# Kernel tuning notes

Measured on AMD Instinct MI355X. Metric: run time of the kernel, lower is better.

The kernel has to match this reference:

```python
import jax, jax.numpy as jnp
import numpy as np

H = 8
NUM_GRAPHS = 128
EDGE_DIM = 147

def _glorot(k, shape, fan_in):
    return jax.random.normal(k, shape, jnp.float32) * (1.0 / np.sqrt(fan_in))

def setup_inputs():
    ks = jax.random.split(jax.random.key(0), 28)
    N, E = 50000, 200000
    inp = {}
    inp['x'] = jax.random.normal(ks[0], (N, 64), jnp.float32)
    inp['edge_attr'] = jax.random.uniform(ks[1], (E, EDGE_DIM), dtype=jnp.float32)
    dims = [(64, 64), (512, 64), (512, 32)]  # (in_channels, per-head out) per GATConv layer
    ki = 2
    for i in range(3):
        cin, c = dims[i]
        hc = H * c
        inp['W%d' % i] = _glorot(ks[ki], (hc, cin), cin); ki += 1
        inp['We%d' % i] = _glorot(ks[ki], (hc, EDGE_DIM), EDGE_DIM); ki += 1
        inp['as%d' % i] = _glorot(ks[ki], (1, H, c), c); ki += 1
        inp['ad%d' % i] = _glorot(ks[ki], (1, H, c), c); ki += 1
        inp['ae%d' % i] = _glorot(ks[ki], (1, H, c), c); ki += 1
        inp['b%d' % i] = jnp.zeros((hc,), jnp.float32); ki += 1
    inp['Wc'] = _glorot(ks[ki], (32, 256), 256)
    inp['bc'] = jnp.zeros((32,), jnp.float32)
    inp['edge_index'] = jax.random.randint(ks[ki + 1], (2, E), 0, N)
    inp['batch'] = jnp.sort(jax.random.randint(ks[ki + 2], (N,), 0, NUM_GRAPHS))
    return inp

def _gat_layer(x, src, dst, ea, W, We, a_s, a_d, a_e, b):
    # PyG GATConv (concat=True, eval mode): project, per-edge attention logits,
    # softmax over incoming edges of each destination node, weighted scatter-sum, bias.
    N = x.shape[0]
    HC = W.shape[0]
    C = HC // H
    xp = (x @ W.T).reshape(N, H, C)              # [N,H,C]
    ep = (ea @ We.T).reshape(-1, H, C)           # [E,H,C]
    logits = (xp * a_s).sum(-1)[src] + (xp * a_d).sum(-1)[dst] + (ep * a_e).sum(-1)
    logits = jax.nn.leaky_relu(logits, 0.2)      # [E,H]
    mx = jax.ops.segment_max(logits, dst, num_segments=N)
    mx = jnp.where(jnp.isfinite(mx), mx, 0.0)
    ex = jnp.exp(logits - mx[dst])
    denom = jax.ops.segment_sum(ex, dst, num_segments=N)
    attn = ex / (denom[dst] + 1e-16)             # [E,H]
    out = jax.ops.segment_sum(xp[src] * attn[:, :, None], dst, num_segments=N)
    return out.reshape(N, HC) + b

def _forward(x, edge_attr, params, Wc, bc, edge_index, batch):
    N = x.shape[0]
    src, dst = edge_index[0], edge_index[1]
    # GATConv add_self_loops=True, fill_value='mean': self-loop edge attr is
    # the per-node mean of incoming edge attrs (0 for isolated nodes).
    ones_e = jnp.ones((src.shape[0],), x.dtype)
    deg = jax.ops.segment_sum(ones_e, dst, num_segments=N)
    loop_attr = jax.ops.segment_sum(edge_attr, dst, num_segments=N) / jnp.clip(deg, 1.0)[:, None]
    ar = jnp.arange(N)
    src_f = jnp.concatenate([src, ar])
    dst_f = jnp.concatenate([dst, ar])
    ea_f = jnp.concatenate([edge_attr, loop_attr], axis=0)
    h = x
    for i, p in enumerate(params):
        h = _gat_layer(h, src_f, dst_f, ea_f, *p)
        if i < len(params) - 1:
            h = jax.nn.elu(h)  # dropout is identity in eval
    # batch indices are sorted and contiguous, so the unique->contiguous remap
    # in the original forward is the identity; global mean pool:
    cnt = jax.ops.segment_sum(jnp.ones((N,), h.dtype), batch, num_segments=NUM_GRAPHS)
    pooled = jax.ops.segment_sum(h, batch, num_segments=NUM_GRAPHS) / jnp.clip(cnt, 1.0)[:, None]
    return pooled @ Wc.T + bc

def reference(x, edge_attr, W0, We0, as0, ad0, ae0, b0, W1, We1, as1, ad1, ae1, b1, W2, We2, as2, ad2, ae2, b2, Wc, bc, edge_index, batch):
    params = [(W0, We0, as0, ad0, ae0, b0), (W1, We1, as1, ad1, ae1, b1), (W2, We2, as2, ad2, ae2, b2)]
    return _forward(x, edge_attr, params, Wc, bc, edge_index, batch)
```

## Files before the change

### kernel.cpp

```cpp
#include <hip/hip_runtime.h>
#include <hip/hip_bf16.h>
#include <math.h>

typedef __attribute__((ext_vector_type(8))) _Float16 f16x8;
typedef __attribute__((ext_vector_type(4))) _Float16 f16x4;
typedef __attribute__((ext_vector_type(4))) float f32x4;

#define AS1(p) ((const __attribute__((address_space(1))) void*)(p))
#define AS3(p) ((__attribute__((address_space(3))) void*)(p))

__device__ __forceinline__ float leaky02(float x){ return x > 0.f ? x : 0.2f*x; }
__device__ __forceinline__ ushort f2h(float f){ _Float16 h = (_Float16)f; return *(ushort*)&h; }
__device__ __forceinline__ float h2f(ushort u){ _Float16 h = *(_Float16*)&u; return (float)h; }

__global__ void count_kernel(const int* __restrict__ dst, int* __restrict__ cnt, int E){
  int e = blockIdx.x*blockDim.x + threadIdx.x;
  if (e < E) atomicAdd(&cnt[dst[e]], 1);
}

__global__ void scanA_kernel(const int* __restrict__ cnt, int* __restrict__ bsum, int N){
  __shared__ int sd[256];
  int i = blockIdx.x*256 + threadIdx.x;
  sd[threadIdx.x] = (i<N) ? cnt[i] : 0;
  __syncthreads();
  for (int off=128; off>0; off>>=1){
    if (threadIdx.x < off) sd[threadIdx.x] += sd[threadIdx.x+off];
    __syncthreads();
  }
  if (threadIdx.x==0) bsum[blockIdx.x] = sd[0];
}
__global__ void scanB_kernel(int* __restrict__ bsum, int B){
  __shared__ int sd[256];
  int t = threadIdx.x;
  int v = (t<B) ? bsum[t] : 0;
  sd[t] = v;
  __syncthreads();
  for (int off=1; off<256; off<<=1){
    int u = (t>=off) ? sd[t-off] : 0;
    __syncthreads();
    sd[t] += u;
    __syncthreads();
  }
  if (t<B) bsum[t] = sd[t] - v;
}
__global__ void scanC_kernel(const int* __restrict__ cnt, const int* __restrict__ bsum,
                             int* __restrict__ row_ptr, int N){
  __shared__ int sd[256];
  int i = blockIdx.x*256 + threadIdx.x;
  int v = (i<N) ? cnt[i] : 0;
  sd[threadIdx.x] = v;
  __syncthreads();
  for (int off=1; off<256; off<<=1){
    int u = (threadIdx.x>=off) ? sd[threadIdx.x-off] : 0;
    __syncthreads();
    sd[threadIdx.x] += u;
    __syncthreads();
  }
  if (i < N) row_ptr[i+1] = sd[threadIdx.x] + bsum[blockIdx.x];
  if (i == 0) row_ptr[0] = 0;
}

__global__ void scatter_kernel(const int* __restrict__ dst, const int* __restrict__ row_ptr,
                               int* __restrict__ cursor, int* __restrict__ csr, int E){
  int e = blockIdx.x*blockDim.x + threadIdx.x;
  if (e < E){
    int d = dst[e];
    int pos = row_ptr[d] + atomicAdd(&cursor[d], 1);
    csr[pos] = e;
  }
}

__global__ void conv4_kernel(const float* __restrict__ p0, const float* __restrict__ p1,
                             const float* __restrict__ p2, const float* __restrict__ p3,
                             ushort* __restrict__ q0, ushort* __restrict__ q1,
                             ushort* __restrict__ q2, ushort* __restrict__ q3,
                             int n0, int n1, int n2, int n3){
  int i = blockIdx.x*256 + threadIdx.x;
  const float* src; ushort* dst; int loc;
  if (i < n0){ src=p0; dst=q0; loc=i; }
  else if (i < n0+n1){ src=p1; dst=q1; loc=i-n0; }
  else if (i < n0+n1+n2){ src=p2; dst=q2; loc=i-n0-n1; }
  else if (i < n0+n1+n2+n3){ src=p3; dst=q3; loc=i-n0-n1-n2; }
  else return;
  float4 v = reinterpret_cast<const float4*>(src)[loc];
  ushort4 o; o.x=f2h(v.x); o.y=f2h(v.y); o.z=f2h(v.z); o.w=f2h(v.w);
  reinterpret_cast<ushort4*>(dst)[loc] = o;
}

__global__ void wfold_direct_kernel(const float* __restrict__ We0, const float* __restrict__ ae0,
                                    const float* __restrict__ We1, const float* __restrict__ ae1,
                                    const float* __restrict__ We2, const float* __restrict__ ae2,
                                    ushort* __restrict__ Bh){
  int t = blockIdx.x*256 + threadIdx.x;
  if (t >= 32*160) return;
  int j = t/160, d = t%160;
  float s = 0.f;
  if (j < 24 && d < 147){
    int l = j >> 3, h = j & 7;
    const float* We = (l==0) ? We0 : (l==1) ? We1 : We2;
    const float* ae = (l==0) ? ae0 : (l==1) ? ae1 : ae2;
    int C = (l==2) ? 32 : 64;
    for (int c=0;c<C;c++) s = fmaf(We[(size_t)(h*C+c)*147 + d], ae[h*C+c], s);
  }
  Bh[t] = f2h(s);
}

__global__ __launch_bounds__(256) void edge_alpha_mfma_kernel(const float* __restrict__ ea, const ushort* __restrict__ Bh,
                                                              float* __restrict__ alphaE, int E){
  int wave = threadIdx.x>>6, lane = threadIdx.x&63;
  int fr = lane&15, fq = lane>>4;
  int m0 = blockIdx.x*64 + wave*16;
  f32x4 acc0 = {0.f,0.f,0.f,0.f}, acc1 = {0.f,0.f,0.f,0.f};
  int row = m0 + fr; if (row > E-1) row = E-1;
  const float*  ar = ea + (size_t)row*147;
  const ushort* b0 = Bh + (size_t)fr*160      + fq*8;
  const ushort* b1 = Bh + (size_t)(16+fr)*160 + fq*8;
  #pragma unroll
  for (int k=0;k<160;k+=32){
    int c0 = k + fq*8;
    f16x8 a;
    #pragma unroll
    for (int u=0;u<8;u++){
      float v = (c0+u < 147) ? ar[c0+u] : 0.f;
      a[u] = (_Float16)v;
    }
    f16x8 p = *(const f16x8*)(b0 + k);
    f16x8 q = *(const f16x8*)(b1 + k);
    acc0 = __builtin_amdgcn_mfma_f32_16x16x32_f16(a, p, acc0, 0, 0, 0);
    acc1 = __builtin_amdgcn_mfma_f32_16x16x32_f16(a, q, acc1, 0, 0, 0);
  }
  #pragma unroll
  for (int j=0;j<4;j++){
    int r = m0 + fq*4 + j;
    if (r < E){
      alphaE[(size_t)r*24 + fr] = acc0[j];
      if (fr < 8) alphaE[(size_t)r*24 + 16 + fr] = acc1[j];
    }
  }
}

__global__ __launch_bounds__(192) void loop_alpha_all_kernel(const float* __restrict__ alphaE, const int* __restrict__ row_ptr,
                                                             const int* __restrict__ csr, float* __restrict__ loopAE, int N){
  int n = blockIdx.x*8 + threadIdx.x/24;
  int j = threadIdx.x%24;
  if (n >= N) return;
  int row = row_ptr[n], end = row_ptr[n+1];
  float s = 0.f;
  for (int i=row;i<end;i++) s += alphaE[(size_t)csr[i]*24 + j];
  loopAE[(size_t)n*24 + j] = s / fmaxf((float)(end-row), 1.0f);
}

template<int CPH>
__global__ __launch_bounds__(256) void gemm_mfma_kernel(const ushort* __restrict__ A, const ushort* __restrict__ B,
                                                        ushort* __restrict__ C,
                                                        const float* __restrict__ a_s, const float* __restrict__ a_d,
                                                        float* __restrict__ alphaS, float* __restrict__ alphaD,
                                                        int M, int Nn, int K, int NY){
  __shared__ ushort lds[128*64*4];
  int nwg = gridDim.x;
  int bid = blockIdx.x;
  int q8 = nwg >> 3, r8 = nwg & 7;
  int xcd = bid & 7, loc = bid >> 3;
  int swz = (xcd < r8 ? xcd*(q8+1) : r8*(q8+1) + (xcd-r8)*q8) + loc;
  int m0 = (swz / NY) * 128, n0 = (swz % NY) * 128;

  int wave = threadIdx.x >> 6, lane = threadIdx.x & 63;
  int wr = wave >> 1, wc = wave & 1;
  f32x4 acc[4][4];
  #pragma unroll
  for (int m=0;m<4;m++)
    #pragma unroll
    for (int n=0;n<4;n++) acc[m][n] = (f32x4){0.f,0.f,0.f,0.f};

  int lrow = lane >> 3;
  int lcol = lane & 7;
  int srcChunk = lcol ^ lrow;
  int fr = lane & 15;
  int fq = lane >> 4;

  auto stage = [&](int buf, int k0){
    ushort* As = lds + buf*(128*64*2);
    ushort* Bs = As + 128*64;
    #pragma unroll
    for (int qq=0;qq<4;qq++){
      int r = qq*32 + wave*8 + lrow;
      int gr = m0 + r; if (gr > M-1) gr = M-1;
      __builtin_amdgcn_global_load_lds(AS1(A + (size_t)gr*K + k0 + srcChunk*8), AS3(&As[(qq*32 + wave*8)*64]), 16, 0, 0);
      __builtin_amdgcn_global_load_lds(AS1(B + (size_t)(n0 + r)*K + k0 + srcChunk*8), AS3(&Bs[(qq*32 + wave*8)*64]), 16, 0, 0);
    }
  };

  int nt = K >> 6;
  stage(0, 0);
  int buf = 0;
  for (int t=0; t<nt; ++t){
    if (t+1 < nt){
      stage(buf^1, (t+1)<<6);
      asm volatile("s_waitcnt vmcnt(8)" ::: "memory");
    } else {
      asm volatile("s_waitcnt vmcnt(0)" ::: "memory");
    }
    __builtin_amdgcn_s_barrier();
    __builtin_amdgcn_sched_barrier(0);
    const ushort* As = lds + buf*(128*64*2);
    const ushort* Bs = As + 128*64;
    #pragma unroll
    for (int kk=0; kk<64; kk+=32){
      f16x8 a[4], b[4];
      #pragma unroll
      for (int m=0;m<4;m++){
        int Ra = wr*64 + m*16 + fr;
        int ch = ((kk>>3) + fq) ^ (Ra & 7);
        a[m] = *(const f16x8*)&As[Ra*64 + ch*8];
      }
      #pragma unroll
      for (int n=0;n<4;n++){
        int Rb = wc*64 + n*16 + fr;
        int ch = ((kk>>3) + fq) ^ (Rb & 7);
        b[n] = *(const f16x8*)&Bs[Rb*64 + ch*8];
      }
      #pragma unroll
      for (int m=0;m<4;m++)
        #pragma unroll
        for (int n=0;n<4;n++)
          acc[m][n] = __builtin_amdgcn_mfma_f32_16x16x32_f16(a[m], b[n], acc[m][n], 0, 0, 0);
    }
    __builtin_amdgcn_s_barrier();
    buf ^= 1;
  }

  {
    ushort* Cs = lds;
    #pragma unroll
    for (int m=0;m<4;m++)
      #pragma unroll
      for (int j=0;j<4;j++){
        int rr = wr*64 + m*16 + fq*4 + j;
        #pragma unroll
        for (int n=0;n<4;n++)
          Cs[rr*128 + wc*64 + n*16 + fr] = f2h(acc[m][n][j]);
      }
    __builtin_amdgcn_s_barrier();
    int rbase = threadIdx.x >> 4;
    int cc = (threadIdx.x & 15)*8;
    #pragma unroll
    for (int p=0;p<8;p++){
      int rr = p*16 + rbase;
      int grow = m0 + rr;
      if (grow < M)
        *(f16x8*)(C + (size_t)grow*Nn + n0 + cc) = *(const f16x8*)&Cs[rr*128 + cc];
    }
  }

  int colbase = n0 + wc*64;
  if (CPH == 64){
    int head = colbase >> 6;
    float asv[4], adv[4];
    #pragma unroll
    for (int n=0;n<4;n++){ int cih = n*16 + fr; asv[n] = a_s[head*64 + cih]; adv[n] = a_d[head*64 + cih]; }
    #pragma unroll
    for (int m=0;m<4;m++){
      float ps[4] = {0,0,0,0}, pd[4] = {0,0,0,0};
      #pragma unroll
      for (int n=0;n<4;n++)
        #pragma unroll
        for (int j=0;j<4;j++){ ps[j] = fmaf(acc[m][n][j], asv[n], ps[j]); pd[j] = fmaf(acc[m][n][j], adv[n], pd[j]); }
      #pragma unroll
      for (int off=1; off<16; off<<=1)
        #pragma unroll
        for (int j=0;j<4;j++){ ps[j] += __shfl_xor(ps[j], off); pd[j] += __shfl_xor(pd[j], off); }
      if (fr == 0){
        #pragma unroll
        for (int j=0;j<4;j++){
          int row = m0 + wr*64 + m*16 + fq*4 + j;
          if (row < M){ alphaS[(size_t)row*8 + head] = ps[j]; alphaD[(size_t)row*8 + head] = pd[j]; }
        }
      }
    }
  } else {
    int head0 = colbase >> 5;
    float asv[4], adv[4];
    #pragma unroll
    for (int n=0;n<4;n++){
      int h = head0 + (n>>1);
      int cih = (n&1)*16 + fr;
      asv[n] = a_s[h*32 + cih]; adv[n] = a_d[h*32 + cih];
    }
    #pragma unroll
    for (int m=0;m<4;m++){
      float psA[4]={0,0,0,0}, pdA[4]={0,0,0,0}, psB[4]={0,0,0,0}, pdB[4]={0,0,0,0};
      #pragma unroll
      for (int j=0;j<4;j++){
        #pragma unroll
        for (int n=0;n<2;n++){ psA[j] = fmaf(acc[m][n][j], asv[n], psA[j]); pdA[j] = fmaf(acc[m][n][j], adv[n], pdA[j]); }
        #pragma unroll
        for (int n=2;n<4;n++){ psB[j] = fmaf(acc[m][n][j], asv[n], psB[j]); pdB[j] = fmaf(acc[m][n][j], adv[n], pdB[j]); }
      }
      #pragma unroll
      for (int off=1; off<16; off<<=1)
        #pragma unroll
        for (int j=0;j<4;j++){
          psA[j] += __shfl_xor(psA[j], off); pdA[j] += __shfl_xor(pdA[j], off);
          psB[j] += __shfl_xor(psB[j], off); pdB[j] += __shfl_xor(pdB[j], off);
        }
      if (fr == 0){
        #pragma unroll
        for (int j=0;j<4;j++){
          int row = m0 + wr*64 + m*16 + fq*4 + j;
          if (row < M){
            alphaS[(size_t)row*8 + head0]     = psA[j]; alphaD[(size_t)row*8 + head0]     = pdA[j];
            alphaS[(size_t)row*8 + head0 + 1] = psB[j]; alphaD[(size_t)row*8 + head0 + 1] = pdB[j];
          }
        }
      }
    }
  }
}

template<int HC, int ELU>
__global__ __launch_bounds__(256) void aggregate_kernel(
    const ushort* __restrict__ xh, const float* __restrict__ alphaS, const float* __restrict__ alphaD,
    const float* __restrict__ alphaE, const float* __restrict__ loopAE,
    const int* __restrict__ row_ptr, const int* __restrict__ csr, const int* __restrict__ src,
    const float* __restrict__ bias, ushort* __restrict__ out, int N){
  constexpr int V = HC/64;
  int n = blockIdx.x*4 + (threadIdx.x>>6);
  if (n >= N) return;
  int lane = threadIdx.x & 63;
  int h = lane >> 3;
  float adn = alphaD[(size_t)n*8 + h];
  float ls = leaky02(alphaS[(size_t)n*8 + h] + adn + loopAE[(size_t)n*24 + h]);
  float ex = __expf(ls);
  float denom = ex;
  float acc[V];
  {
    const ushort* xr = xh + (size_t)n*HC + V*lane;
    if (V == 8){
      f16x8 v = *(const f16x8*)xr;
      #pragma unroll
      for (int j=0;j<8;j++) acc[j] = ex * (float)v[j];
    } else {
      f16x4 v = *(const f16x4*)xr;
      #pragma unroll
      for (int j=0;j<V;j++) acc[j] = ex * (float)v[j];
    }
  }
  int i = row_ptr[n], i1 = row_ptr[n+1];
  for (; i+1 < i1; i += 2){
    int e0 = csr[i], e1 = csr[i+1];
    int s0 = src[e0], s1 = src[e1];
    float aS0 = alphaS[(size_t)s0*8 + h], aE0 = alphaE[(size_t)e0*24 + h];
    float aS1 = alphaS[(size_t)s1*8 + h], aE1 = alphaE[(size_t)e1*24 + h];
    const ushort* x0 = xh + (size_t)s0*HC + V*lane;
    const ushort* x1 = xh + (size_t)s1*HC + V*lane;
    if (V == 8){
      f16x8 v0 = *(const f16x8*)x0;
      f16x8 v1 = *(const f16x8*)x1;
      float ex0 = __expf(leaky02(aS0 + adn + aE0));
      float ex1 = __expf(leaky02(aS1 + adn + aE1));
      denom += ex0 + ex1;
      #pragma unroll
      for (int j=0;j<8;j++) acc[j] = fmaf(ex1, (float)v1[j], fmaf(ex0, (float)v0[j], acc[j]));
    } else {
      f16x4 v0 = *(const f16x4*)x0;
      f16x4 v1 = *(const f16x4*)x1;
      float ex0 = __expf(leaky02(aS0 + adn + aE0));
      float ex1 = __expf(leaky02(aS1 + adn + aE1));
      denom += ex0 + ex1;
      #pragma unroll
      for (int j=0;j<V;j++) acc[j] = fmaf(ex1, (float)v1[j], fmaf(ex0, (float)v0[j], acc[j]));
    }
  }
  if (i < i1){
    int e = csr[i]; int s = src[e];
    float t = leaky02(alphaS[(size_t)s*8 + h] + adn + alphaE[(size_t)e*24 + h]);
    float exv = __expf(t);
    denom += exv;
    const ushort* xs = xh + (size_t)s*HC + V*lane;
    if (V == 8){
      f16x8 v = *(const f16x8*)xs;
      #pragma unroll
      for (int j=0;j<8;j++) acc[j] = fmaf(exv, (float)v[j], acc[j]);
    } else {
      f16x4 v = *(const f16x4*)xs;
      #pragma unroll
      for (int j=0;j<V;j++) acc[j] = fmaf(exv, (float)v[j], acc[j]);
    }
  }
  float inv = 1.f/(denom + 1e-16f);
  if (V == 8){
    f16x8 ov;
    #pragma unroll
    for (int j=0;j<8;j++){
      float o = acc[j]*inv + bias[V*lane + j];
      if (ELU) o = (o > 0.f) ? o : expm1f(o);
      ov[j] = (_Float16)o;
    }
    *(f16x8*)(out + (size_t)n*HC + V*lane) = ov;
  } else {
    f16x4 ov;
    #pragma unroll
    for (int j=0;j<V;j++){
      float o = acc[j]*inv + bias[V*lane + j];
      if (ELU) o = (o > 0.f) ? o : expm1f(o);
      ov[j] = (_Float16)o;
    }
    *(f16x4*)(out + (size_t)n*HC + V*lane) = ov;
  }
}

__global__ __launch_bounds__(256) void pool_sum_kernel(const ushort* __restrict__ h, const int* __restrict__ batch,
                                                       float* __restrict__ pooled, int N){
  __shared__ int bsh[128];
  int i0 = blockIdx.x*128;
  int i1 = min(i0+128, N);
  if (threadIdx.x < i1-i0) bsh[threadIdx.x] = batch[i0+threadIdx.x];
  __syncthreads();
  int c = threadIdx.x;
  int gprev = bsh[0];
  float s = 0.f;
  for (int i=i0;i<i1;i++){
    int g = bsh[i-i0];
    if (g != gprev){ atomicAdd(&pooled[gprev*256 + c], s); s = 0.f; gprev = g; }
    s += h2f(h[(size_t)i*256 + c]);
  }
  atomicAdd(&pooled[gprev*256 + c], s);
}

__device__ __forceinline__ int lower_bound_i(const int* a, int n, int key){
  int lo=0, hi=n;
  while (lo<hi){ int mid=(lo+hi)>>1; if (a[mid]<key) lo=mid+1; else hi=mid; }
  return lo;
}

__global__ void final_kernel(const float* __restrict__ pooled, const int* __restrict__ batch,
                             const float* __restrict__ Wc, const float* __restrict__ bc,
                             float* __restrict__ out, int N){
  int g = blockIdx.x; int j = threadIdx.x;
  if (j >= 32) return;
  int start = lower_bound_i(batch, N, g);
  int end   = lower_bound_i(batch, N, g+1);
  float invc = 1.f / fmaxf((float)(end-start), 1.f);
  const float* p = pooled + g*256;
  const float* w = Wc + (size_t)j*256;
  float s = 0.f;
  for (int c=0;c<256;c++) s = fmaf(p[c], w[c], s);
  out[g*32 + j] = s*invc + bc[j];
}

extern "C" void kernel_launch(void* const* d_in, const int* in_sizes, int n_in,
                              void* d_out, int out_size, void* d_ws, size_t ws_size,
                              hipStream_t stream){
  (void)n_in; (void)out_size; (void)ws_size;
  const float* x   = (const float*)d_in[0];
  const float* ea  = (const float*)d_in[1];
  const float* Wt[3]  = {(const float*)d_in[2],  (const float*)d_in[8],  (const float*)d_in[14]};
  const float* Wet[3] = {(const float*)d_in[3],  (const float*)d_in[9],  (const float*)d_in[15]};
  const float* ast[3] = {(const float*)d_in[4],  (const float*)d_in[10], (const float*)d_in[16]};
  const float* adt[3] = {(const float*)d_in[5],  (const float*)d_in[11], (const float*)d_in[17]};
  const float* aet[3] = {(const float*)d_in[6],  (const float*)d_in[12], (const float*)d_in[18]};
  const float* bt[3]  = {(const float*)d_in[7],  (const float*)d_in[13], (const float*)d_in[19]};
  const float* Wc  = (const float*)d_in[20];
  const float* bc  = (const float*)d_in[21];
  const int* ei    = (const int*)d_in[22];
  const int* batch = (const int*)d_in[23];
  int N = in_sizes[0] / 64;
  int E = in_sizes[1] / 147;
  const int* srcp = ei;
  const int* dstp = ei + E;

  char* w = (char*)d_ws;
  size_t off = 0;
  auto carve = [&](size_t bytes)->char*{ char* p = w + off; off += (bytes + 255) & ~(size_t)255; return p; };
  ushort* xh     = (ushort*)carve((size_t)N*512*2);
  ushort* hb     = (ushort*)carve((size_t)N*512*2);
  ushort* xb     = (ushort*)carve((size_t)N*64*2);
  ushort* Wb[3];
  Wb[0] = (ushort*)carve((size_t)512*64*2);
  Wb[1] = (ushort*)carve((size_t)512*512*2);
  Wb[2] = (ushort*)carve((size_t)256*512*2);
  ushort* wfBh   = (ushort*)carve((size_t)32*160*2);
  float*  alphaE = (float*) carve((size_t)E*24*4);
  float*  loopAE = (float*) carve((size_t)N*24*4);
  float*  alphaS = (float*) carve((size_t)N*8*4);
  float*  alphaD = (float*) carve((size_t)N*8*4);
  int*    row_ptr= (int*)   carve((size_t)(N+1)*4);
  int*    csr    = (int*)   carve((size_t)E*4);
  int*    bsum   = (int*)   carve((size_t)256*4);
  char*   zbase  = carve(0);
  float*  pooled = (float*) carve((size_t)128*256*4);
  int*    cnt    = (int*)   carve((size_t)N*4);
  int*    cursor = (int*)   carve((size_t)N*4);
  char*   zend   = carve(0);

  hipMemsetAsync(zbase, 0, (size_t)(zend - zbase), stream);

  int nscan = (N+255)/256;
  count_kernel  <<<(E+255)/256, 256, 0, stream>>>(dstp, cnt, E);
  scanA_kernel  <<<nscan, 256, 0, stream>>>(cnt, bsum, N);
  scanB_kernel  <<<1, 256, 0, stream>>>(bsum, nscan);
  scanC_kernel  <<<nscan, 256, 0, stream>>>(cnt, bsum, row_ptr, N);
  scatter_kernel<<<(E+255)/256, 256, 0, stream>>>(dstp, row_ptr, cursor, csr, E);

  wfold_direct_kernel<<<(32*160+255)/256, 256, 0, stream>>>(Wet[0], aet[0], Wet[1], aet[1], Wet[2], aet[2], wfBh);

  conv4_kernel<<<(N*16 + 8192 + 65536 + 32768 + 255)/256, 256, 0, stream>>>(
      x, Wt[0], Wt[1], Wt[2], xb, Wb[0], Wb[1], Wb[2], N*16, 8192, 65536, 32768);

  edge_alpha_mfma_kernel<<<(E+63)/64, 256, 0, stream>>>(ea, wfBh, alphaE, E);
  loop_alpha_all_kernel <<<(N+7)/8, 192, 0, stream>>>(alphaE, row_ptr, csr, loopAE, N);

  const int HCs[3]  = {512, 512, 256};
  const int CINs[3] = {64, 512, 512};
  int nrow = (N+127)/128;
  for (int l=0; l<3; l++){
    int HC = HCs[l], CIN = CINs[l];
    const ushort* Ain = (l==0) ? xb : hb;
    int NY = HC/128;
    int nwg = nrow * NY;
    if (HC==512) gemm_mfma_kernel<64><<<nwg, 256, 0, stream>>>(Ain, Wb[l], xh, ast[l], adt[l], alphaS, alphaD, N, HC, CIN, NY);
    else         gemm_mfma_kernel<32><<<nwg, 256, 0, stream>>>(Ain, Wb[l], xh, ast[l], adt[l], alphaS, alphaD, N, HC, CIN, NY);
    int ablocks = (N + 3) / 4;
    if (l==0)
      aggregate_kernel<512,1><<<ablocks, 256, 0, stream>>>(xh, alphaS, alphaD, alphaE + 0*8, loopAE + 0*8, row_ptr, csr, srcp, bt[l], hb, N);
    else if (l==1)
      aggregate_kernel<512,1><<<ablocks, 256, 0, stream>>>(xh, alphaS, alphaD, alphaE + 1*8, loopAE + 1*8, row_ptr, csr, srcp, bt[l], hb, N);
    else
      aggregate_kernel<256,0><<<ablocks, 256, 0, stream>>>(xh, alphaS, alphaD, alphaE + 2*8, loopAE + 2*8, row_ptr, csr, srcp, bt[l], hb, N);
  }
  pool_sum_kernel<<<(N+127)/128, 256, 0, stream>>>(hb, batch, pooled, N);
  final_kernel<<<128, 64, 0, stream>>>(pooled, batch, Wc, bc, (float*)d_out, N);
}
```

Baseline: 476.7 us.

## Store edge attention in CSR order and precompute per-edge exponentials

The scatter step now records each edge's CSR position and writes the source and destination ids in CSR order. The edge-alpha kernel writes its results straight into CSR order, so the loop-attribute and aggregation kernels read contiguous data instead of following csr→edge indirection. A new per-layer edge_exp kernel computes the leaky-ReLU plus exp for every edge and self loop before aggregation, so the aggregate kernel only loads these values. The cost is an extra kernel launch per layer and an E×8 float buffer written and read each layer, while scattered writes move into the edge-alpha kernel.

New measurement: 487.7 us. 2.3% more time.

```diff
diff --git a/kernel.cpp b/kernel.cpp
--- a/kernel.cpp
+++ b/kernel.cpp
@@ -60,13 +60,17 @@
   if (i == 0) row_ptr[0] = 0;
 }
 
-__global__ void scatter_kernel(const int* __restrict__ dst, const int* __restrict__ row_ptr,
-                               int* __restrict__ cursor, int* __restrict__ csr, int E){
+__global__ void scatter_kernel(const int* __restrict__ src, const int* __restrict__ dst,
+                               const int* __restrict__ row_ptr, int* __restrict__ cursor,
+                               int* __restrict__ epos, int* __restrict__ csr_src,
+                               int* __restrict__ csr_dst, int E){
   int e = blockIdx.x*blockDim.x + threadIdx.x;
   if (e < E){
     int d = dst[e];
     int pos = row_ptr[d] + atomicAdd(&cursor[d], 1);
-    csr[pos] = e;
+    epos[e] = pos;
+    csr_src[pos] = src[e];
+    csr_dst[pos] = d;
   }
 }
 
@@ -106,7 +110,8 @@
 }
 
 __global__ __launch_bounds__(256) void edge_alpha_mfma_kernel(const float* __restrict__ ea, const ushort* __restrict__ Bh,
-                                                              float* __restrict__ alphaE, int E){
+                                                              const int* __restrict__ epos,
+                                                              float* __restrict__ aEc, int E){
   int wave = threadIdx.x>>6, lane = threadIdx.x&63;
   int fr = lane&15, fq = lane>>4;
   int m0 = blockIdx.x*64 + wave*16;
@@ -133,21 +138,42 @@
   for (int j=0;j<4;j++){
     int r = m0 + fq*4 + j;
     if (r < E){
-      alphaE[(size_t)r*24 + fr] = acc0[j];
-      if (fr < 8) alphaE[(size_t)r*24 + 16 + fr] = acc1[j];
-    }
-  }
-}
-
-__global__ __launch_bounds__(192) void loop_alpha_all_kernel(const float* __restrict__ alphaE, const int* __restrict__ row_ptr,
-                                                             const int* __restrict__ csr, float* __restrict__ loopAE, int N){
+      int p = epos[r];
+      aEc[(size_t)p*24 + fr] = acc0[j];
+      if (fr < 8) aEc[(size_t)p*24 + 16 + fr] = acc1[j];
+    }
+  }
+}
+
+__global__ __launch_bounds__(192) void loop_alpha_all_kernel(const float* __restrict__ aEc, const int* __restrict__ row_ptr,
+                                                             float* __restrict__ loopAE, int N){
   int n = blockIdx.x*8 + threadIdx.x/24;
   int j = threadIdx.x%24;
   if (n >= N) return;
   int row = row_ptr[n], end = row_ptr[n+1];
   float s = 0.f;
-  for (int i=row;i<end;i++) s += alphaE[(size_t)csr[i]*24 + j];
+  for (int i=row;i<end;i++) s += aEc[(size_t)i*24 + j];
   loopAE[(size_t)n*24 + j] = s / fmaxf((float)(end-row), 1.0f);
+}
+
+__global__ __launch_bounds__(256) void edge_exp_kernel(
+    const float* __restrict__ alphaS, const float* __restrict__ alphaD,
+    const float* __restrict__ aEc, const float* __restrict__ loopAE,
+    const int* __restrict__ csr_src, const int* __restrict__ csr_dst,
+    float* __restrict__ exv_csr, float* __restrict__ selfEx,
+    int E, int N, int off){
+  int t = blockIdx.x*256 + threadIdx.x;
+  if (t < E*8){
+    int i = t >> 3, h = t & 7;
+    int s = csr_src[i], n = csr_dst[i];
+    float v = leaky02(alphaS[(size_t)s*8+h] + alphaD[(size_t)n*8+h] + aEc[(size_t)i*24 + off + h]);
+    exv_csr[t] = __expf(v);
+  } else if (t < (E+N)*8){
+    int u = t - E*8;
+    int n = u >> 3, h = u & 7;
+    float v = leaky02(alphaS[(size_t)n*8+h] + alphaD[(size_t)n*8+h] + loopAE[(size_t)n*24 + off + h]);
+    selfEx[u] = __expf(v);
+  }
 }
 
 template<int CPH>
@@ -319,18 +345,15 @@
 
 template<int HC, int ELU>
 __global__ __launch_bounds__(256) void aggregate_kernel(
-    const ushort* __restrict__ xh, const float* __restrict__ alphaS, const float* __restrict__ alphaD,
-    const float* __restrict__ alphaE, const float* __restrict__ loopAE,
-    const int* __restrict__ row_ptr, const int* __restrict__ csr, const int* __restrict__ src,
+    const ushort* __restrict__ xh, const float* __restrict__ exv_csr, const float* __restrict__ selfEx,
+    const int* __restrict__ row_ptr, const int* __restrict__ csr_src,
     const float* __restrict__ bias, ushort* __restrict__ out, int N){
   constexpr int V = HC/64;
   int n = blockIdx.x*4 + (threadIdx.x>>6);
   if (n >= N) return;
   int lane = threadIdx.x & 63;
   int h = lane >> 3;
-  float adn = alphaD[(size_t)n*8 + h];
-  float ls = leaky02(alphaS[(size_t)n*8 + h] + adn + loopAE[(size_t)n*24 + h]);
-  float ex = __expf(ls);
+  float ex = selfEx[(size_t)n*8 + h];
   float denom = ex;
   float acc[V];
   {
@@ -347,34 +370,27 @@
   }
   int i = row_ptr[n], i1 = row_ptr[n+1];
   for (; i+1 < i1; i += 2){
-    int e0 = csr[i], e1 = csr[i+1];
-    int s0 = src[e0], s1 = src[e1];
-    float aS0 = alphaS[(size_t)s0*8 + h], aE0 = alphaE[(size_t)e0*24 + h];
-    float aS1 = alphaS[(size_t)s1*8 + h], aE1 = alphaE[(size_t)e1*24 + h];
+    int s0 = csr_src[i], s1 = csr_src[i+1];
+    float ex0 = exv_csr[(size_t)i*8 + h];
+    float ex1 = exv_csr[(size_t)(i+1)*8 + h];
     const ushort* x0 = xh + (size_t)s0*HC + V*lane;
     const ushort* x1 = xh + (size_t)s1*HC + V*lane;
+    denom += ex0 + ex1;
     if (V == 8){
       f16x8 v0 = *(const f16x8*)x0;
       f16x8 v1 = *(const f16x8*)x1;
-      float ex0 = __expf(leaky02(aS0 + adn + aE0));
-      float ex1 = __expf(leaky02(aS1 + adn + aE1));
-      denom += ex0 + ex1;
       #pragma unroll
       for (int j=0;j<8;j++) acc[j] = fmaf(ex1, (float)v1[j], fmaf(ex0, (float)v0[j], acc[j]));
     } else {
       f16x4 v0 = *(const f16x4*)x0;
       f16x4 v1 = *(const f16x4*)x1;
-      float ex0 = __expf(leaky02(aS0 + adn + aE0));
-      float ex1 = __expf(leaky02(aS1 + adn + aE1));
-      denom += ex0 + ex1;
       #pragma unroll
       for (int j=0;j<V;j++) acc[j] = fmaf(ex1, (float)v1[j], fmaf(ex0, (float)v0[j], acc[j]));
     }
   }
   if (i < i1){
-    int e = csr[i]; int s = src[e];
-    float t = leaky02(alphaS[(size_t)s*8 + h] + adn + alphaE[(size_t)e*24 + h]);
-    float exv = __expf(t);
+    int s = csr_src[i];
+    float exv = exv_csr[(size_t)i*8 + h];
     denom += exv;
     const ushort* xs = xh + (size_t)s*HC + V*lane;
     if (V == 8){
@@ -480,12 +496,16 @@
   Wb[1] = (ushort*)carve((size_t)512*512*2);
   Wb[2] = (ushort*)carve((size_t)256*512*2);
   ushort* wfBh   = (ushort*)carve((size_t)32*160*2);
-  float*  alphaE = (float*) carve((size_t)E*24*4);
+  float*  aEc    = (float*) carve((size_t)E*24*4);
   float*  loopAE = (float*) carve((size_t)N*24*4);
   float*  alphaS = (float*) carve((size_t)N*8*4);
   float*  alphaD = (float*) carve((size_t)N*8*4);
+  float*  exv    = (float*) carve((size_t)E*8*4);
+  float*  selfEx = (float*) carve((size_t)N*8*4);
   int*    row_ptr= (int*)   carve((size_t)(N+1)*4);
-  int*    csr    = (int*)   carve((size_t)E*4);
+  int*    epos   = (int*)   carve((size_t)E*4);
+  int*    csr_src= (int*)   carve((size_t)E*4);
+  int*    csr_dst= (int*)   carve((size_t)E*4);
   int*    bsum   = (int*)   carve((size_t)256*4);
   char*   zbase  = carve(0);
   float*  pooled = (float*) carve((size_t)128*256*4);
@@ -500,19 +520,20 @@
   scanA_kernel  <<<nscan, 256, 0, stream>>>(cnt, bsum, N);
   scanB_kernel  <<<1, 256, 0, stream>>>(bsum, nscan);
   scanC_kernel  <<<nscan, 256, 0, stream>>>(cnt, bsum, row_ptr, N);
-  scatter_kernel<<<(E+255)/256, 256, 0, stream>>>(dstp, row_ptr, cursor, csr, E);
+  scatter_kernel<<<(E+255)/256, 256, 0, stream>>>(srcp, dstp, row_ptr, cursor, epos, csr_src, csr_dst, E);
 
   wfold_direct_kernel<<<(32*160+255)/256, 256, 0, stream>>>(Wet[0], aet[0], Wet[1], aet[1], Wet[2], aet[2], wfBh);
 
   conv4_kernel<<<(N*16 + 8192 + 65536 + 32768 + 255)/256, 256, 0, stream>>>(
       x, Wt[0], Wt[1], Wt[2], xb, Wb[0], Wb[1], Wb[2], N*16, 8192, 65536, 32768);
 
-  edge_alpha_mfma_kernel<<<(E+63)/64, 256, 0, stream>>>(ea, wfBh, alphaE, E);
-  loop_alpha_all_kernel <<<(N+7)/8, 192, 0, stream>>>(alphaE, row_ptr, csr, loopAE, N);
+  edge_alpha_mfma_kernel<<<(E+63)/64, 256, 0, stream>>>(ea, wfBh, epos, aEc, E);
+  loop_alpha_all_kernel <<<(N+7)/8, 192, 0, stream>>>(aEc, row_ptr, loopAE, N);
 
   const int HCs[3]  = {512, 512, 256};
   const int CINs[3] = {64, 512, 512};
   int nrow = (N+127)/128;
+  int nexp = ((E+N)*8 + 255)/256;
   for (int l=0; l<3; l++){
     int HC = HCs[l], CIN = CINs[l];
     const ushort* Ain = (l==0) ? xb : hb;
@@ -520,13 +541,14 @@
     int nwg = nrow * NY;
     if (HC==512) gemm_mfma_kernel<64><<<nwg, 256, 0, stream>>>(Ain, Wb[l], xh, ast[l], adt[l], alphaS, alphaD, N, HC, CIN, NY);
     else         gemm_mfma_kernel<32><<<nwg, 256, 0, stream>>>(Ain, Wb[l], xh, ast[l], adt[l], alphaS, alphaD, N, HC, CIN, NY);
+    edge_exp_kernel<<<nexp, 256, 0, stream>>>(alphaS, alphaD, aEc, loopAE, csr_src, csr_dst, exv, selfEx, E, N, l*8);
     int ablocks = (N + 3) / 4;
     if (l==0)
-      aggregate_kernel<512,1><<<ablocks, 256, 0, stream>>>(xh, alphaS, alphaD, alphaE + 0*8, loopAE + 0*8, row_ptr, csr, srcp, bt[l], hb, N);
+      aggregate_kernel<512,1><<<ablocks, 256, 0, stream>>>(xh, exv, selfEx, row_ptr, csr_src, bt[l], hb, N);
     else if (l==1)
-      aggregate_kernel<512,1><<<ablocks, 256, 0, stream>>>(xh, alphaS, alphaD, alphaE + 1*8, loopAE + 1*8, row_ptr, csr, srcp, bt[l], hb, N);
+      aggregate_kernel<512,1><<<ablocks, 256, 0, stream>>>(xh, exv, selfEx, row_ptr, csr_src, bt[l], hb, N);
     else
-      aggregate_kernel<256,0><<<ablocks, 256, 0, stream>>>(xh, alphaS, alphaD, alphaE + 2*8, loopAE + 2*8, row_ptr, csr, srcp, bt[l], hb, N);
+      aggregate_kernel<256,0><<<ablocks, 256, 0, stream>>>(xh, exv, selfEx, row_ptr, csr_src, bt[l], hb, N);
   }
   pool_sum_kernel<<<(N+127)/128, 256, 0, stream>>>(hb, batch, pooled, N);
   final_kernel<<<128, 64, 0, stream>>>(pooled, batch, Wc, bc, (float*)d_out, N);
```
